# Performance work log

Measured on AMD Instinct MI355X. Metric: run time of the kernel, lower is better.

## Reference

```python
import jax, jax.numpy as jnp
import numpy as np

B, S, D, H, O = 8, 4096, 512, 512, 512
NS, NC, SD = 4, 4, 8
CLIP, TEMP, SUP_SCALE, SUP_EPS, LN_EPS = 3.0, 1.0, 1.0, 1e-4, 1e-5


def _ln(x, w, b):
    m = jnp.mean(x, -1, keepdims=True)
    v = jnp.mean((x - m) ** 2, -1, keepdims=True)
    return (x - m) * jax.lax.rsqrt(v + LN_EPS) * w + b


def _lin(x, w, b):
    return x @ w.T + b


def setup_inputs() -> dict:
    key = jax.random.key(0)
    ks = iter(jax.random.split(key, 32))

    def W(shape):
        return 0.02 * jax.random.normal(next(ks), shape, jnp.float32)

    inp = {}
    inp['x'] = jax.random.normal(next(ks), (B, S, D), jnp.float32)
    inp['sb_norm_w'] = jnp.ones((D,), jnp.float32)
    inp['sb_norm_b'] = jnp.zeros((D,), jnp.float32)
    inp['sb_proj_w'] = W((NS, D)); inp['sb_proj_b'] = jnp.zeros((NS,), jnp.float32)
    inp['sb_sum_w'] = W((SD, 4)); inp['sb_sum_b'] = jnp.zeros((SD,), jnp.float32)
    inp['cb_norm_w'] = jnp.ones((D,), jnp.float32)
    inp['cb_norm_b'] = jnp.zeros((D,), jnp.float32)
    inp['cb_proj_w'] = W((NC, D)); inp['cb_proj_b'] = jnp.zeros((NC,), jnp.float32)
    inp['cb_sum_w'] = W((SD, 4)); inp['cb_sum_b'] = jnp.zeros((SD,), jnp.float32)
    inp['vn_norm_w'] = jnp.ones((D,), jnp.float32)
    inp['vn_norm_b'] = jnp.zeros((D,), jnp.float32)
    inp['vn_w1'] = W((H, D)); inp['vn_b1'] = jnp.zeros((H,), jnp.float32)
    inp['vn_w2'] = W((O, H)); inp['vn_b2'] = jnp.zeros((O,), jnp.float32)
    inp['un_norm_w'] = jnp.ones((D,), jnp.float32)
    inp['un_norm_b'] = jnp.zeros((D,), jnp.float32)
    inp['un_w1'] = W((H, D)); inp['un_b1'] = jnp.zeros((H,), jnp.float32)
    inp['un_w2'] = W((1, H)); inp['un_b2'] = jnp.zeros((1,), jnp.float32)
    inp['en_w'] = W((H, 1)); inp['en_b'] = jnp.zeros((H,), jnp.float32)
    inp['pr_w'] = W((H, 1)); inp['pr_b'] = jnp.zeros((H,), jnp.float32)
    inp['rs_w'] = W((H, 1)); inp['rs_b'] = jnp.zeros((H,), jnp.float32)
    inp['ssp_w'] = W((H, SD)); inp['ssp_b'] = jnp.zeros((H,), jnp.float32)
    inp['csp_w'] = W((H, SD)); inp['csp_b'] = jnp.zeros((H,), jnp.float32)
    inp['out_w'] = W((O, O + 5 * H)); inp['out_b'] = jnp.zeros((O,), jnp.float32)
    inp['support_logits'] = jnp.zeros((NS,), jnp.float32)
    inp['conflict_weights'] = jnp.ones((NC,), jnp.float32)
    inp['drive_bias'] = jnp.zeros((1,), jnp.float32)
    inp['bias_resistance'] = jnp.zeros((1,), jnp.float32)
    inp['update_threshold'] = jnp.ones((1,), jnp.float32)
    inp['eml_gamma'] = jnp.full((1,), 0.3, jnp.float32)
    inp['eml_lambda'] = jnp.ones((1,), jnp.float32)
    inp['eml_bias'] = jnp.zeros((1,), jnp.float32)
    return inp


def reference(x, sb_norm_w, sb_norm_b, sb_proj_w, sb_proj_b, sb_sum_w, sb_sum_b,
              cb_norm_w, cb_norm_b, cb_proj_w, cb_proj_b, cb_sum_w, cb_sum_b,
              vn_norm_w, vn_norm_b, vn_w1, vn_b1, vn_w2, vn_b2,
              un_norm_w, un_norm_b, un_w1, un_b1, un_w2, un_b2,
              en_w, en_b, pr_w, pr_b, rs_w, rs_b,
              ssp_w, ssp_b, csp_w, csp_b, out_w, out_b,
              support_logits, conflict_weights, drive_bias, bias_resistance,
              update_threshold, eml_gamma, eml_lambda, eml_bias):
    # Support bank: LN -> Linear -> softplus(+eps) -> stats -> summary Linear
    sf = jax.nn.softplus(_lin(_ln(x, sb_norm_w, sb_norm_b), sb_proj_w, sb_proj_b)) + SUP_EPS  # [B,S,NS]
    ls = jnp.log(sf)
    s_seed = jnp.concatenate([
        sf.mean(-1, keepdims=True), sf.std(-1, keepdims=True),
        ls.mean(-1, keepdims=True), ls.max(-1, keepdims=True)], -1)
    ss = _lin(s_seed, sb_sum_w, sb_sum_b)  # [B,S,SD]
    # Conflict bank
    cf = jax.nn.softplus(_lin(_ln(x, cb_norm_w, cb_norm_b), cb_proj_w, cb_proj_b))  # [B,S,NC]
    c_seed = jnp.concatenate([
        cf.mean(-1, keepdims=True), cf.std(-1, keepdims=True),
        cf.max(-1, keepdims=True), cf.min(-1, keepdims=True)], -1)
    cs = _lin(c_seed, cb_sum_w, cb_sum_b)  # [B,S,SD]
    # Drive / resistance
    sw = jax.nn.softmax(support_logits)
    drive = drive_bias + SUP_SCALE * (ls * sw).sum(-1, keepdims=True) / np.sqrt(NS)
    cw = jax.nn.softplus(conflict_weights)
    weighted_conflict = (cf * cw).sum(-1, keepdims=True) / np.sqrt(NC)
    u_h = jax.nn.gelu(_lin(_ln(x, un_norm_w, un_norm_b), un_w1, un_b1), approximate=False)
    uncertainty = jax.nn.softplus(_lin(u_h, un_w2, un_b2))  # [B,S,1]
    resistance = bias_resistance + weighted_conflict + uncertainty
    # EML unit (dim=1): bounded linear drive-resistance balance, warmup_eta=1.0
    e_raw = eml_gamma * drive - eml_lambda * resistance + eml_bias
    energy = CLIP * jnp.tanh(e_raw / CLIP)
    activation = jax.nn.sigmoid(energy / TEMP)
    precision = jax.nn.softplus(energy - update_threshold)
    # Value net
    v_h = jax.nn.gelu(_lin(_ln(x, vn_norm_w, vn_norm_b), vn_w1, vn_b1), approximate=False)
    value = _lin(v_h, vn_w2, vn_b2)  # [B,S,O]
    feats = jnp.concatenate([
        activation * value,
        _lin(energy, en_w, en_b),
        _lin(precision, pr_w, pr_b),
        _lin(resistance, rs_w, rs_b),
        _lin(ss, ssp_w, ssp_b),
        _lin(cs, csp_w, csp_b)], -1)  # [B,S,O+5H]
    return _lin(feats, out_w, out_b)  # [B,S,O]
```

## Files before the change

kernel.cpp:

```cpp
#include <hip/hip_runtime.h>
#include <stdint.h>

typedef unsigned short u16;
typedef __bf16 bf16x8 __attribute__((ext_vector_type(8)));
typedef float f32x4 __attribute__((ext_vector_type(4)));
typedef __attribute__((address_space(1))) void gvoid;
typedef __attribute__((address_space(3))) void lvoid;

#define NTOK 32768

#define FENCE() asm volatile("" ::: "memory")
#define SBAR()  do { FENCE(); __builtin_amdgcn_s_barrier(); FENCE(); } while (0)
#define SVM4()  asm volatile("s_waitcnt vmcnt(4)" ::: "memory")
#define SVM0()  asm volatile("s_waitcnt vmcnt(0)" ::: "memory")

__device__ __forceinline__ u16 f2bf(float f) {
    unsigned u = __float_as_uint(f);
    u += 0x7fffu + ((u >> 16) & 1u);
    return (u16)(u >> 16);
}
__device__ __forceinline__ float softplusf(float x) {
    return fmaxf(x, 0.f) + log1pf(expf(-fabsf(x)));
}
__device__ __forceinline__ float geluf(float x) {
    return 0.5f * x * (1.f + erff(x * 0.7071067811865475f));
}
__device__ __forceinline__ float wave_sum(float v) {
#pragma unroll
    for (int o = 32; o > 0; o >>= 1) v += __shfl_xor(v, o);
    return v;
}
__device__ __forceinline__ float blk_sum(float v) {
    __shared__ float sm[4];
    v = wave_sum(v);
    __syncthreads();
    if ((threadIdx.x & 63) == 0) sm[threadIdx.x >> 6] = v;
    __syncthreads();
    return sm[0] + sm[1] + sm[2] + sm[3];
}

__global__ void k_fold(
    const float* __restrict__ vnw1, const float* __restrict__ vnnw, const float* __restrict__ vnnb, const float* __restrict__ vnb1,
    const float* __restrict__ unw1, const float* __restrict__ unnw, const float* __restrict__ unnb, const float* __restrict__ unb1,
    const float* __restrict__ sbpw, const float* __restrict__ sbpb, const float* __restrict__ sbnw, const float* __restrict__ sbnb,
    const float* __restrict__ cbpw, const float* __restrict__ cbpb, const float* __restrict__ cbnw, const float* __restrict__ cbnb,
    const float* __restrict__ outw, const float* __restrict__ enw, const float* __restrict__ enb,
    const float* __restrict__ prw, const float* __restrict__ prb,
    const float* __restrict__ rsw, const float* __restrict__ rsb,
    const float* __restrict__ sspw, const float* __restrict__ sspb,
    const float* __restrict__ cspw, const float* __restrict__ cspb,
    const float* __restrict__ vnw2, const float* __restrict__ vnb2,
    u16* __restrict__ Astk, float* __restrict__ bstk, float* __restrict__ pb,
    u16* __restrict__ Aow, u16* __restrict__ vnT,
    float* __restrict__ a_en, float* __restrict__ a_pr, float* __restrict__ a_rs,
    float* __restrict__ b_vo, float* __restrict__ c_cn, float* __restrict__ Mss, float* __restrict__ Mcs)
{
    const int b = blockIdx.x, t = threadIdx.x;
    if (b < 1024) {
        const float *w1, *nw, *nb; float bias;
        if (b < 512) { w1 = vnw1 + (size_t)b * 512; nw = vnnw; nb = vnnb; bias = vnb1[b]; }
        else { int r = b - 512; w1 = unw1 + (size_t)r * 512; nw = unnw; nb = unnb; bias = unb1[r]; }
        float part = 0.f;
        for (int d = t; d < 512; d += 256) {
            float wv = w1[d];
            Astk[(size_t)b * 512 + d] = f2bf(wv * nw[d]);
            part += wv * nb[d];
        }
        float s = blk_sum(part);
        if (t == 0) bstk[b] = bias + s;
    } else if (b < 1032) {
        int j = b - 1024;
        const float *pw, *nw, *nb; float bias;
        if (j < 4) { pw = sbpw + j * 512; nw = sbnw; nb = sbnb; bias = sbpb[j]; }
        else { pw = cbpw + (j - 4) * 512; nw = cbnw; nb = cbnb; bias = cbpb[j - 4]; }
        float part = 0.f;
        for (int d = t; d < 512; d += 256) {
            float wv = pw[d];
            Astk[(size_t)(1024 + j) * 512 + d] = f2bf(wv * nw[d]);
            part += wv * nb[d];
        }
        float s = blk_sum(part);
        if (t == 0) pb[j] = bias + s;
    } else if (b < 1152) {
        for (int d = t; d < 512; d += 256) Astk[(size_t)b * 512 + d] = 0;
    } else if (b < 1664) {
        int i = b - 1152;
        const float* ow = outw + (size_t)i * 3072;
        float pen = 0, ppr = 0, prs = 0, pbv = 0, pcc = 0;
        float pms[8], pmc[8];
#pragma unroll
        for (int k = 0; k < 8; k++) { pms[k] = 0.f; pmc[k] = 0.f; }
        for (int h = t; h < 512; h += 256) {
            float o0 = ow[h];        Aow[(size_t)i * 512 + h] = f2bf(o0); pbv += o0 * vnb2[h];
            float o1 = ow[512 + h];  pen += o1 * enw[h]; pcc += o1 * enb[h];
            float o2 = ow[1024 + h]; ppr += o2 * prw[h]; pcc += o2 * prb[h];
            float o3 = ow[1536 + h]; prs += o3 * rsw[h]; pcc += o3 * rsb[h];
            float o4 = ow[2048 + h]; pcc += o4 * sspb[h];
            float o5 = ow[2560 + h]; pcc += o5 * cspb[h];
#pragma unroll
            for (int k = 0; k < 8; k++) { pms[k] += o4 * sspw[h * 8 + k]; pmc[k] += o5 * cspw[h * 8 + k]; }
        }
        float r;
        r = blk_sum(pen); if (t == 0) a_en[i] = r;
        r = blk_sum(ppr); if (t == 0) a_pr[i] = r;
        r = blk_sum(prs); if (t == 0) a_rs[i] = r;
        r = blk_sum(pbv); if (t == 0) b_vo[i] = r;
        r = blk_sum(pcc); if (t == 0) c_cn[i] = r;
        for (int k = 0; k < 8; k++) { r = blk_sum(pms[k]); if (t == 0) Mss[i * 8 + k] = r; }
        for (int k = 0; k < 8; k++) { r = blk_sum(pmc[k]); if (t == 0) Mcs[i * 8 + k] = r; }
    } else {
        int hrow = b - 1664;
        for (int o = t; o < 512; o += 256)
            vnT[(size_t)hrow * 512 + o] = f2bf(vnw2[(size_t)o * 512 + hrow]);
    }
}

__device__ __forceinline__ void load_bfrag8(const u16* bufB, bf16x8 (&bfrag)[4][2], int wn, int l) {
#pragma unroll
    for (int nt = 0; nt < 4; nt++) {
        const int row = wn * 64 + nt * 16 + (l & 15);
#pragma unroll
        for (int ks = 0; ks < 2; ks++) {
            const int s = (ks * 4 + (l >> 4)) ^ (row & 7);
            bfrag[nt][ks] = *(const bf16x8*)(bufB + row * 64 + (s << 3));
        }
    }
}

template <int Q>
__device__ __forceinline__ void load_aquad8(const u16* bufA, bf16x8 (&af)[2], int wm, int l) {
    const int row = wm * 64 + Q * 16 + (l & 15);
#pragma unroll
    for (int ks = 0; ks < 2; ks++) {
        const int s = (ks * 4 + (l >> 4)) ^ (row & 7);
        af[ks] = *(const bf16x8*)(bufA + row * 64 + (s << 3));
    }
}

template <int Q>
__device__ __forceinline__ void do_mfma8(bf16x8 (&af)[2], bf16x8 (&bfrag)[4][2], f32x4 (&acc)[4][4]) {
#pragma unroll
    for (int nt = 0; nt < 4; nt++)
#pragma unroll
        for (int ks = 0; ks < 2; ks++)
            acc[Q][nt] = __builtin_amdgcn_mfma_f32_16x16x32_bf16(af[ks], bfrag[nt][ks], acc[Q][nt], 0, 0, 0);
}

#define PHASE8(Q, bufA_, bufB_, READB, STAGE_STMT, VM_STMT)       \
    do {                                                          \
        if (READB) load_bfrag8(bufB_, bfrag, wn, l);              \
        bf16x8 af[2];                                             \
        load_aquad8<Q>(bufA_, af, wm, l);                         \
        STAGE_STMT;                                               \
        SBAR();                                                   \
        __builtin_amdgcn_s_setprio(1);                            \
        do_mfma8<Q>(af, bfrag, acc);                              \
        __builtin_amdgcn_s_setprio(0);                            \
        VM_STMT;                                                  \
        SBAR();                                                   \
    } while (0)

__device__ __forceinline__ void gemm8_mainloop(const u16* __restrict__ Ag, const u16* __restrict__ Bg,
                                               size_t arow0, size_t brow0,
                                               u16* sm, f32x4 (&acc)[4][4], int w, int l)
{
    const int wm = w >> 1, wn = w & 1;
    u16* const sA0 = sm;
    u16* const sA1 = sm + 8192;
    u16* const sB0 = sm + 16384;
    u16* const sB1 = sm + 24576;
    const int rchunk = l >> 3;
    const int gc = (((l & 7) ^ ((l >> 3) & 7)) << 3);

    auto STG = [&](const u16* g, size_t rb, int tile, u16* lbase) {
        const int kt = tile * 64;
#pragma unroll
        for (int i = 0; i < 4; i++) {
            const int r0 = (w * 4 + i) * 8;
            __builtin_amdgcn_global_load_lds(
                (gvoid*)const_cast<u16*>(g + (rb + r0 + rchunk) * 512 + kt + gc),
                (lvoid*)(lbase + r0 * 64), 16, 0, 0);
        }
    };

    STG(Ag, arow0, 0, sA0);
    STG(Bg, brow0, 0, sB0);
    STG(Bg, brow0, 1, sB1);
    SVM4();
    SBAR();

    bf16x8 bfrag[4][2];
    for (int it = 0; it < 4; ++it) {
        const int t1 = 2 * it + 1, t2 = 2 * it + 2, t3 = 2 * it + 3;
        const bool lastit = (it == 3);
        PHASE8(0, sA0, sB0, true,  { STG(Ag, arow0, t1, sA1); }, );
        PHASE8(1, sA0, sB0, false, { if (t2 < 8) STG(Bg, brow0, t2, sB0); }, );
        PHASE8(2, sA0, sB0, false, { }, );
        PHASE8(3, sA0, sB0, false, { }, { if (lastit) { SVM0(); } else { SVM4(); } });
        PHASE8(0, sA1, sB1, true,  { if (t2 < 8) STG(Ag, arow0, t2, sA0); }, );
        PHASE8(1, sA1, sB1, false, { if (t3 < 8) STG(Bg, brow0, t3, sB1); }, );
        PHASE8(2, sA1, sB1, false, { }, );
        PHASE8(3, sA1, sB1, false, { }, { SVM4(); });
    }
}

__device__ __forceinline__ void gt_stage(const u16* __restrict__ A_, int lda,
                                         const u16* __restrict__ B_, int ldb, int kt,
                                         u16* dA, u16* dB, int w, int lrow, int lcol)
{
#pragma unroll
    for (int i = 0; i < 4; i++) {
        const int chunk = i * 4 + w;
        const int row = chunk * 8 + lrow;
        __builtin_amdgcn_global_load_lds((gvoid*)const_cast<u16*>(A_ + (size_t)row * lda + kt + lcol),
                                         (lvoid*)(dA + chunk * 512), 16, 0, 0);
        __builtin_amdgcn_global_load_lds((gvoid*)const_cast<u16*>(B_ + (size_t)row * ldb + kt + lcol),
                                         (lvoid*)(dB + chunk * 512), 16, 0, 0);
    }
}
__device__ __forceinline__ void gt_compute(const u16* lA, const u16* lB, f32x4 (&acc)[4][4],
                                           int wr, int wc, int frow, int fk, int sw)
{
#pragma unroll
    for (int ks = 0; ks < 2; ks++) {
        bf16x8 af[4], bfv[4];
        const int c = (ks * 32 + fk);
#pragma unroll
        for (int rt = 0; rt < 4; rt++)
            af[rt] = *(const bf16x8*)(lA + (wr + rt * 16 + frow) * 64 + (c ^ sw));
#pragma unroll
        for (int ct = 0; ct < 4; ct++)
            bfv[ct] = *(const bf16x8*)(lB + (wc + ct * 16 + frow) * 64 + (c ^ sw));
#pragma unroll
        for (int rt = 0; rt < 4; rt++)
#pragma unroll
            for (int ct = 0; ct < 4; ct++)
                acc[rt][ct] = __builtin_amdgcn_mfma_f32_16x16x32_bf16(af[rt], bfv[ct], acc[rt][ct], 0, 0, 0);
    }
}
__device__ __forceinline__ void gemm_tile(const u16* __restrict__ Ab, int lda,
                                          const u16* __restrict__ Bb, int ldb,
                                          int K, u16* sm, f32x4 (&acc)[4][4])
{
    const int t = threadIdx.x;
    const int w = t >> 6, l = t & 63;
    const int lrow = l >> 3;
    const int lcol = ((l ^ (((l >> 3) & 3) << 1)) & 7) * 8;
    const int wr = ((w >> 1) << 6), wc = ((w & 1) << 6);
    const int frow = l & 15, fk = ((l >> 4) << 3);
    const int sw = (frow & 3) << 4;
    u16* lA0 = sm;          u16* lA1 = sm + 8192;
    u16* lB0 = sm + 16384;  u16* lB1 = sm + 24576;
    gt_stage(Ab, lda, Bb, ldb, 0, lA0, lB0, w, lrow, lcol);
    __syncthreads();
    for (int kt = 0; kt < K; kt += 128) {
        if (kt + 64 < K) gt_stage(Ab, lda, Bb, ldb, kt + 64, lA1, lB1, w, lrow, lcol);
        gt_compute(lA0, lB0, acc, wr, wc, frow, fk, sw);
        __syncthreads();
        if (kt + 128 < K) gt_stage(Ab, lda, Bb, ldb, kt + 128, lA0, lB0, w, lrow, lcol);
        gt_compute(lA1, lB1, acc, wr, wc, frow, fk, sw);
        __syncthreads();
    }
}

__global__ __launch_bounds__(256, 2) void k_gemm_wvo(const u16* __restrict__ A, const u16* __restrict__ Bm,
                                                     u16* __restrict__ C)
{
    __shared__ __align__(16) u16 smem[32768];
    const f32x4 zero = {0.f, 0.f, 0.f, 0.f};
    f32x4 acc[4][4];
#pragma unroll
    for (int a = 0; a < 4; a++)
#pragma unroll
        for (int c = 0; c < 4; c++) acc[a][c] = zero;
    const u16* Ab = A + (size_t)blockIdx.y * 128 * 512;
    const u16* Bb = Bm + (size_t)blockIdx.x * 128 * 512;
    gemm_tile(Ab, 512, Bb, 512, 512, smem, acc);
    const int t = threadIdx.x, w = t >> 6, l = t & 63;
    const int rbase = blockIdx.y * 128 + ((w >> 1) << 6);
    const int cbase = blockIdx.x * 128 + ((w & 1) << 6);
    const int lr = ((l >> 4) << 2), lc = l & 15;
#pragma unroll
    for (int rt = 0; rt < 4; rt++)
#pragma unroll
        for (int ct = 0; ct < 4; ct++)
#pragma unroll
            for (int j = 0; j < 4; j++)
                C[(size_t)(rbase + rt * 16 + lr + j) * 512 + cbase + ct * 16 + lc] = f2bf(acc[rt][ct][j]);
}

__global__ void k_token(const float* __restrict__ x, u16* __restrict__ Ybf)
{
    const int w = threadIdx.x >> 6, l = threadIdx.x & 63;
    const int n = blockIdx.x * 4 + w;
    const float* xr = x + (size_t)n * 512;
    float4 xa = *(const float4*)(xr + 4 * l);
    float4 xb = *(const float4*)(xr + 256 + 4 * l);
    float v[8] = {xa.x, xa.y, xa.z, xa.w, xb.x, xb.y, xb.z, xb.w};
    float s1 = 0.f, s2 = 0.f;
#pragma unroll
    for (int c = 0; c < 8; c++) { s1 += v[c]; s2 += v[c] * v[c]; }
    s1 = wave_sum(s1); s2 = wave_sum(s2);
    const float mean = s1 * (1.f / 512.f);
    const float var = s2 * (1.f / 512.f) - mean * mean;
    const float rstd = rsqrtf(var + 1e-5f);
    float y[8];
#pragma unroll
    for (int c = 0; c < 8; c++) y[c] = (v[c] - mean) * rstd;
    *(ushort4*)(Ybf + (size_t)n * 512 + 4 * l) = make_ushort4(f2bf(y[0]), f2bf(y[1]), f2bf(y[2]), f2bf(y[3]));
    *(ushort4*)(Ybf + (size_t)n * 512 + 256 + 4 * l) = make_ushort4(f2bf(y[4]), f2bf(y[5]), f2bf(y[6]), f2bf(y[7]));
}

__global__ __launch_bounds__(256, 2) void k_gemm1(const u16* __restrict__ Y, const u16* __restrict__ Ast,
                                                  const float* __restrict__ bstk, const float* __restrict__ pb,
                                                  const float* __restrict__ unw2,
                                                  u16* __restrict__ H, float* __restrict__ wp,
                                                  float* __restrict__ wdotp)
{
    __shared__ __align__(16) u16 smem[32768];
    const f32x4 zero = {0.f, 0.f, 0.f, 0.f};
    f32x4 acc[4][4];
#pragma unroll
    for (int a = 0; a < 4; a++)
#pragma unroll
        for (int c = 0; c < 4; c++) acc[a][c] = zero;
    const int nwg = gridDim.x * gridDim.y;
    const int lin = blockIdx.y * gridDim.x + blockIdx.x;
    const int swz = (lin & 7) * (nwg >> 3) + (lin >> 3);
    const int by = swz / gridDim.x, bx = swz % gridDim.x;
    const int t = threadIdx.x, w = t >> 6, l = t & 63;

    gemm8_mainloop(Y, Ast, (size_t)by * 128, (size_t)bx * 128, smem, acc, w, l);

    const int wr = ((w >> 1) << 6), wc = ((w & 1) << 6);
    const int lr = ((l >> 4) << 2), lc = l & 15;
    if (bx == 8) {
        if ((w & 1) == 0 && lc < 8) {
            const float bv = pb[lc];
            const int rbase = by * 128 + wr;
#pragma unroll
            for (int rt = 0; rt < 4; rt++)
#pragma unroll
                for (int j = 0; j < 4; j++) {
                    const int n = rbase + rt * 16 + lr + j;
                    wp[(size_t)n * 8 + lc] = acc[rt][0][j] + bv;
                }
        }
        return;
    }
    if (bx >= 4) {
        const int cb = (bx - 4) * 128;
        float part[4][4];
#pragma unroll
        for (int rt = 0; rt < 4; rt++)
#pragma unroll
            for (int j = 0; j < 4; j++) part[rt][j] = 0.f;
#pragma unroll
        for (int ct = 0; ct < 4; ct++) {
            const int col = cb + wc + ct * 16 + lc;
            const float bv = bstk[512 + col];
            const float w2 = unw2[col];
#pragma unroll
            for (int rt = 0; rt < 4; rt++)
#pragma unroll
                for (int j = 0; j < 4; j++)
                    part[rt][j] += geluf(acc[rt][ct][j] + bv) * w2;
        }
        float* sf = (float*)smem;
        const int slot = ((w & 1) << 4) | lc;
        __syncthreads();
#pragma unroll
        for (int rt = 0; rt < 4; rt++)
#pragma unroll
            for (int j = 0; j < 4; j++)
                sf[(wr + rt * 16 + lr + j) * 32 + slot] = part[rt][j];
        __syncthreads();
        if (t < 128) {
            float s = 0.f;
#pragma unroll
            for (int k2 = 0; k2 < 32; k2++) s += sf[t * 32 + k2];
            wdotp[(size_t)(bx - 4) * NTOK + by * 128 + t] = s;
        }
        return;
    }
    __syncthreads();
#pragma unroll
    for (int ct = 0; ct < 4; ct++) {
        const int col = wc + ct * 16 + lc;
        const float bv = bstk[bx * 128 + col];
#pragma unroll
        for (int rt = 0; rt < 4; rt++) {
            const int row = wr + rt * 16 + lr;
#pragma unroll
            for (int j = 0; j < 4; j++)
                smem[(row + j) * 136 + col] = f2bf(geluf(acc[rt][ct][j] + bv));
        }
    }
    __syncthreads();
    const size_t gbase = (size_t)(by * 128) * 512 + bx * 128;
#pragma unroll
    for (int jj = 0; jj < 8; jj++) {
        const int r = jj * 16 + (t >> 4), u = t & 15;
        bf16x8 vv = *(const bf16x8*)(smem + r * 136 + u * 8);
        *(bf16x8*)(H + gbase + (size_t)r * 512 + u * 8) = vv;
    }
}

__global__ void k_bank(const float* __restrict__ wp, const float* __restrict__ wdotp,
                       const float* __restrict__ unb2,
                       const float* __restrict__ sbsw, const float* __restrict__ sbsb,
                       const float* __restrict__ cbsw, const float* __restrict__ cbsb,
                       const float* __restrict__ suplog, const float* __restrict__ confw,
                       const float* __restrict__ drvb, const float* __restrict__ biasres,
                       const float* __restrict__ emlg, const float* __restrict__ emll,
                       const float* __restrict__ emlb, const float* __restrict__ updthr,
                       float* __restrict__ wss, float* __restrict__ wcs, float* __restrict__ wsc)
{
    const int n = blockIdx.x * 256 + threadIdx.x;
    float4 p0 = *(const float4*)(wp + (size_t)n * 8);
    float4 p1 = *(const float4*)(wp + (size_t)n * 8 + 4);
    float p[8] = {p0.x, p0.y, p0.z, p0.w, p1.x, p1.y, p1.z, p1.w};
    const float dot = wdotp[n] + wdotp[NTOK + n] + wdotp[2 * NTOK + n] + wdotp[3 * NTOK + n];
    float sf[4], lsv[4], cf[4];
#pragma unroll
    for (int j = 0; j < 4; j++) {
        sf[j] = softplusf(p[j]) + 1e-4f;
        lsv[j] = logf(sf[j]);
        cf[j] = softplusf(p[j + 4]);
    }
    const float smn = 0.25f * (sf[0] + sf[1] + sf[2] + sf[3]);
    float sd = 0.f;
#pragma unroll
    for (int j = 0; j < 4; j++) sd += (sf[j] - smn) * (sf[j] - smn);
    const float sstd = sqrtf(0.25f * sd);
    const float lmn = 0.25f * (lsv[0] + lsv[1] + lsv[2] + lsv[3]);
    const float lmx = fmaxf(fmaxf(lsv[0], lsv[1]), fmaxf(lsv[2], lsv[3]));
    const float cmn = 0.25f * (cf[0] + cf[1] + cf[2] + cf[3]);
    float cd = 0.f;
#pragma unroll
    for (int j = 0; j < 4; j++) cd += (cf[j] - cmn) * (cf[j] - cmn);
    const float cstd = sqrtf(0.25f * cd);
    const float cmx = fmaxf(fmaxf(cf[0], cf[1]), fmaxf(cf[2], cf[3]));
    const float cmi = fminf(fminf(cf[0], cf[1]), fminf(cf[2], cf[3]));
    float seed_s[4] = {smn, sstd, lmn, lmx};
    float seed_c[4] = {cmn, cstd, cmx, cmi};
    float a4[8], b4[8];
#pragma unroll
    for (int k = 0; k < 8; k++) {
        float a = sbsb[k], b2 = cbsb[k];
#pragma unroll
        for (int j = 0; j < 4; j++) { a += sbsw[k * 4 + j] * seed_s[j]; b2 += cbsw[k * 4 + j] * seed_c[j]; }
        a4[k] = a; b4[k] = b2;
    }
    *(float4*)(wss + (size_t)n * 8)     = make_float4(a4[0], a4[1], a4[2], a4[3]);
    *(float4*)(wss + (size_t)n * 8 + 4) = make_float4(a4[4], a4[5], a4[6], a4[7]);
    *(float4*)(wcs + (size_t)n * 8)     = make_float4(b4[0], b4[1], b4[2], b4[3]);
    *(float4*)(wcs + (size_t)n * 8 + 4) = make_float4(b4[4], b4[5], b4[6], b4[7]);
    float mx = fmaxf(fmaxf(suplog[0], suplog[1]), fmaxf(suplog[2], suplog[3]));
    float e[4], se = 0.f;
#pragma unroll
    for (int j = 0; j < 4; j++) { e[j] = expf(suplog[j] - mx); se += e[j]; }
    float dv = 0.f, wcv = 0.f;
#pragma unroll
    for (int j = 0; j < 4; j++) { dv += lsv[j] * (e[j] / se); wcv += cf[j] * softplusf(confw[j]); }
    const float drive = drvb[0] + 0.5f * dv;
    const float unc = softplusf(dot + unb2[0]);
    const float res = biasres[0] + 0.5f * wcv + unc;
    const float er = emlg[0] * drive - emll[0] * res + emlb[0];
    const float energy = 3.f * tanhf(er * (1.f / 3.f));
    const float act = 1.f / (1.f + expf(-energy));
    const float prc = softplusf(energy - updthr[0]);
    wsc[(size_t)n * 4 + 0] = act;
    wsc[(size_t)n * 4 + 1] = energy;
    wsc[(size_t)n * 4 + 2] = prc;
    wsc[(size_t)n * 4 + 3] = res;
}

__global__ __launch_bounds__(256, 2) void k_gemm2(const u16* __restrict__ H, const u16* __restrict__ Wvo,
    const float* __restrict__ wsc, const float* __restrict__ wss, const float* __restrict__ wcs,
    const float* __restrict__ a_en, const float* __restrict__ a_pr, const float* __restrict__ a_rs,
    const float* __restrict__ b_vo, const float* __restrict__ c_cn,
    const float* __restrict__ Mss, const float* __restrict__ Mcs,
    const float* __restrict__ outb, float* __restrict__ out)
{
    __shared__ __align__(16) u16 smem[32768];
    const f32x4 zero = {0.f, 0.f, 0.f, 0.f};
    f32x4 acc[4][4];
#pragma unroll
    for (int a = 0; a < 4; a++)
#pragma unroll
        for (int c = 0; c < 4; c++) acc[a][c] = zero;
    const int nwg = gridDim.x * gridDim.y;
    const int lin = blockIdx.y * gridDim.x + blockIdx.x;
    const int swz = (lin & 7) * (nwg >> 3) + (lin >> 3);
    const int by = swz / gridDim.x, bx = swz % gridDim.x;
    const int t = threadIdx.x, w = t >> 6, l = t & 63;

    gemm8_mainloop(H, Wvo, (size_t)by * 128, (size_t)bx * 128, smem, acc, w, l);

    const int rbase = by * 128 + ((w >> 1) << 6);
    const int cbase = bx * 128 + ((w & 1) << 6);
    const int lr = ((l >> 4) << 2), lc = l & 15;
    float bvo4[4], aen4[4], apr4[4], ars4[4], cc4[4], ms4[4][8], mc4[4][8];
#pragma unroll
    for (int ct = 0; ct < 4; ct++) {
        const int i = cbase + ct * 16 + lc;
        bvo4[ct] = b_vo[i]; aen4[ct] = a_en[i]; apr4[ct] = a_pr[i]; ars4[ct] = a_rs[i];
        cc4[ct] = c_cn[i] + outb[i];
#pragma unroll
        for (int k = 0; k < 8; k++) { ms4[ct][k] = Mss[i * 8 + k]; mc4[ct][k] = Mcs[i * 8 + k]; }
    }
#pragma unroll
    for (int rt = 0; rt < 4; rt++)
#pragma unroll
        for (int j = 0; j < 4; j++) {
            const int n = rbase + rt * 16 + lr + j;
            const float act = wsc[(size_t)n * 4 + 0];
            const float eng = wsc[(size_t)n * 4 + 1];
            const float prc = wsc[(size_t)n * 4 + 2];
            const float res = wsc[(size_t)n * 4 + 3];
            float sv[8], cv[8];
#pragma unroll
            for (int k = 0; k < 8; k++) { sv[k] = wss[(size_t)n * 8 + k]; cv[k] = wcs[(size_t)n * 8 + k]; }
#pragma unroll
            for (int ct = 0; ct < 4; ct++) {
                const int i = cbase + ct * 16 + lc;
                float o = act * (acc[rt][ct][j] + bvo4[ct]) + eng * aen4[ct] + prc * apr4[ct]
                        + res * ars4[ct] + cc4[ct];
#pragma unroll
                for (int k = 0; k < 8; k++) o += ms4[ct][k] * sv[k] + mc4[ct][k] * cv[k];
                out[(size_t)n * 512 + i] = o;
            }
        }
}

extern "C" void kernel_launch(void* const* d_in, const int* in_sizes, int n_in,
                              void* d_out, int out_size, void* d_ws, size_t ws_size,
                              hipStream_t stream)
{
    const float* x       = (const float*)d_in[0];
    const float* sbnw    = (const float*)d_in[1];
    const float* sbnb    = (const float*)d_in[2];
    const float* sbpw    = (const float*)d_in[3];
    const float* sbpb    = (const float*)d_in[4];
    const float* sbsw    = (const float*)d_in[5];
    const float* sbsb    = (const float*)d_in[6];
    const float* cbnw    = (const float*)d_in[7];
    const float* cbnb    = (const float*)d_in[8];
    const float* cbpw    = (const float*)d_in[9];
    const float* cbpb    = (const float*)d_in[10];
    const float* cbsw    = (const float*)d_in[11];
    const float* cbsb    = (const float*)d_in[12];
    const float* vnnw    = (const float*)d_in[13];
    const float* vnnb    = (const float*)d_in[14];
    const float* vnw1    = (const float*)d_in[15];
    const float* vnb1    = (const float*)d_in[16];
    const float* vnw2    = (const float*)d_in[17];
    const float* vnb2    = (const float*)d_in[18];
    const float* unnw    = (const float*)d_in[19];
    const float* unnb    = (const float*)d_in[20];
    const float* unw1    = (const float*)d_in[21];
    const float* unb1    = (const float*)d_in[22];
    const float* unw2    = (const float*)d_in[23];
    const float* unb2    = (const float*)d_in[24];
    const float* enw     = (const float*)d_in[25];
    const float* enb     = (const float*)d_in[26];
    const float* prw     = (const float*)d_in[27];
    const float* prb     = (const float*)d_in[28];
    const float* rsw     = (const float*)d_in[29];
    const float* rsb     = (const float*)d_in[30];
    const float* sspw    = (const float*)d_in[31];
    const float* sspb    = (const float*)d_in[32];
    const float* cspw    = (const float*)d_in[33];
    const float* cspb    = (const float*)d_in[34];
    const float* outw    = (const float*)d_in[35];
    const float* outb    = (const float*)d_in[36];
    const float* suplog  = (const float*)d_in[37];
    const float* confw   = (const float*)d_in[38];
    const float* drvb    = (const float*)d_in[39];
    const float* biasres = (const float*)d_in[40];
    const float* updthr  = (const float*)d_in[41];
    const float* emlg    = (const float*)d_in[42];
    const float* emll    = (const float*)d_in[43];
    const float* emlb    = (const float*)d_in[44];
    float* out = (float*)d_out;
    (void)in_sizes; (void)n_in; (void)out_size; (void)ws_size;

    char* wsp = (char*)d_ws;
    size_t off = 0;
    auto alloc = [&](size_t bytes) { char* p = wsp + off; off = (off + bytes + 255) & ~(size_t)255; return p; };
    u16*  Ybf  = (u16*)alloc((size_t)NTOK * 512 * 2);
    u16*  Hbf  = (u16*)alloc((size_t)NTOK * 512 * 2);
    u16*  Astk = (u16*)alloc(1152 * 512 * 2);
    float* bstk = (float*)alloc(1024 * 4);
    float* pb   = (float*)alloc(8 * 4);
    u16*  Aow  = (u16*)alloc(512 * 512 * 2);
    u16*  vnT  = (u16*)alloc(512 * 512 * 2);
    u16*  Wvo  = (u16*)alloc(512 * 512 * 2);
    float* a_en = (float*)alloc(512 * 4);
    float* a_pr = (float*)alloc(512 * 4);
    float* a_rs = (float*)alloc(512 * 4);
    float* b_vo = (float*)alloc(512 * 4);
    float* c_cn = (float*)alloc(512 * 4);
    float* Mss  = (float*)alloc(512 * 8 * 4);
    float* Mcs  = (float*)alloc(512 * 8 * 4);
    float* wp   = (float*)alloc((size_t)NTOK * 8 * 4);
    float* wdotp= (float*)alloc((size_t)NTOK * 4 * 4);
    float* wss  = (float*)alloc((size_t)NTOK * 8 * 4);
    float* wcs  = (float*)alloc((size_t)NTOK * 8 * 4);
    float* wsc  = (float*)alloc((size_t)NTOK * 4 * 4);

    k_fold<<<2176, 256, 0, stream>>>(vnw1, vnnw, vnnb, vnb1, unw1, unnw, unnb, unb1,
                                     sbpw, sbpb, sbnw, sbnb, cbpw, cbpb, cbnw, cbnb,
                                     outw, enw, enb, prw, prb, rsw, rsb, sspw, sspb, cspw, cspb,
                                     vnw2, vnb2,
                                     Astk, bstk, pb, Aow, vnT, a_en, a_pr, a_rs, b_vo, c_cn, Mss, Mcs);
    k_gemm_wvo<<<dim3(4, 4), 256, 0, stream>>>(Aow, vnT, Wvo);
    k_token<<<NTOK / 4, 256, 0, stream>>>(x, Ybf);
    k_gemm1<<<dim3(9, 256), 256, 0, stream>>>(Ybf, Astk, bstk, pb, unw2, Hbf, wp, wdotp);
    k_bank<<<NTOK / 256, 256, 0, stream>>>(wp, wdotp, unb2, sbsw, sbsb, cbsw, cbsb,
                                           suplog, confw, drvb, biasres, emlg, emll, emlb, updthr,
                                           wss, wcs, wsc);
    k_gemm2<<<dim3(4, 256), 256, 0, stream>>>(Hbf, Wvo, wsc, wss, wcs, a_en, a_pr, a_rs, b_vo, c_cn,
                                              Mss, Mcs, outb, out);
}
```

Before: 154.1 us.

## Fuse Wvo weight GEMM into gemm1 grid and bank math into gemm2 prologue

The small Wvo = Aow·vnT GEMM becomes an extra grid column in k_gemm1 (bx==9, 16 active blocks), and the separate k_bank kernel is dropped. Its per-token math is recomputed into shared memory at the start of each k_gemm2 block. This removes two kernel launches and the global round-trip of the wss/wcs/wsc intermediates. In exchange, the bank computation is done redundantly by each of the 4 column blocks, 240 extra blocks launch and exit at once, and k_gemm2 uses more LDS, which could reduce occupancy.

```diff
diff --git a/kernel.cpp b/kernel.cpp
--- a/kernel.cpp
+++ b/kernel.cpp
@@ -204,91 +204,6 @@
     }
 }
 
-__device__ __forceinline__ void gt_stage(const u16* __restrict__ A_, int lda,
-                                         const u16* __restrict__ B_, int ldb, int kt,
-                                         u16* dA, u16* dB, int w, int lrow, int lcol)
-{
-#pragma unroll
-    for (int i = 0; i < 4; i++) {
-        const int chunk = i * 4 + w;
-        const int row = chunk * 8 + lrow;
-        __builtin_amdgcn_global_load_lds((gvoid*)const_cast<u16*>(A_ + (size_t)row * lda + kt + lcol),
-                                         (lvoid*)(dA + chunk * 512), 16, 0, 0);
-        __builtin_amdgcn_global_load_lds((gvoid*)const_cast<u16*>(B_ + (size_t)row * ldb + kt + lcol),
-                                         (lvoid*)(dB + chunk * 512), 16, 0, 0);
-    }
-}
-__device__ __forceinline__ void gt_compute(const u16* lA, const u16* lB, f32x4 (&acc)[4][4],
-                                           int wr, int wc, int frow, int fk, int sw)
-{
-#pragma unroll
-    for (int ks = 0; ks < 2; ks++) {
-        bf16x8 af[4], bfv[4];
-        const int c = (ks * 32 + fk);
-#pragma unroll
-        for (int rt = 0; rt < 4; rt++)
-            af[rt] = *(const bf16x8*)(lA + (wr + rt * 16 + frow) * 64 + (c ^ sw));
-#pragma unroll
-        for (int ct = 0; ct < 4; ct++)
-            bfv[ct] = *(const bf16x8*)(lB + (wc + ct * 16 + frow) * 64 + (c ^ sw));
-#pragma unroll
-        for (int rt = 0; rt < 4; rt++)
-#pragma unroll
-            for (int ct = 0; ct < 4; ct++)
-                acc[rt][ct] = __builtin_amdgcn_mfma_f32_16x16x32_bf16(af[rt], bfv[ct], acc[rt][ct], 0, 0, 0);
-    }
-}
-__device__ __forceinline__ void gemm_tile(const u16* __restrict__ Ab, int lda,
-                                          const u16* __restrict__ Bb, int ldb,
-                                          int K, u16* sm, f32x4 (&acc)[4][4])
-{
-    const int t = threadIdx.x;
-    const int w = t >> 6, l = t & 63;
-    const int lrow = l >> 3;
-    const int lcol = ((l ^ (((l >> 3) & 3) << 1)) & 7) * 8;
-    const int wr = ((w >> 1) << 6), wc = ((w & 1) << 6);
-    const int frow = l & 15, fk = ((l >> 4) << 3);
-    const int sw = (frow & 3) << 4;
-    u16* lA0 = sm;          u16* lA1 = sm + 8192;
-    u16* lB0 = sm + 16384;  u16* lB1 = sm + 24576;
-    gt_stage(Ab, lda, Bb, ldb, 0, lA0, lB0, w, lrow, lcol);
-    __syncthreads();
-    for (int kt = 0; kt < K; kt += 128) {
-        if (kt + 64 < K) gt_stage(Ab, lda, Bb, ldb, kt + 64, lA1, lB1, w, lrow, lcol);
-        gt_compute(lA0, lB0, acc, wr, wc, frow, fk, sw);
-        __syncthreads();
-        if (kt + 128 < K) gt_stage(Ab, lda, Bb, ldb, kt + 128, lA0, lB0, w, lrow, lcol);
-        gt_compute(lA1, lB1, acc, wr, wc, frow, fk, sw);
-        __syncthreads();
-    }
-}
-
-__global__ __launch_bounds__(256, 2) void k_gemm_wvo(const u16* __restrict__ A, const u16* __restrict__ Bm,
-                                                     u16* __restrict__ C)
-{
-    __shared__ __align__(16) u16 smem[32768];
-    const f32x4 zero = {0.f, 0.f, 0.f, 0.f};
-    f32x4 acc[4][4];
-#pragma unroll
-    for (int a = 0; a < 4; a++)
-#pragma unroll
-        for (int c = 0; c < 4; c++) acc[a][c] = zero;
-    const u16* Ab = A + (size_t)blockIdx.y * 128 * 512;
-    const u16* Bb = Bm + (size_t)blockIdx.x * 128 * 512;
-    gemm_tile(Ab, 512, Bb, 512, 512, smem, acc);
-    const int t = threadIdx.x, w = t >> 6, l = t & 63;
-    const int rbase = blockIdx.y * 128 + ((w >> 1) << 6);
-    const int cbase = blockIdx.x * 128 + ((w & 1) << 6);
-    const int lr = ((l >> 4) << 2), lc = l & 15;
-#pragma unroll
-    for (int rt = 0; rt < 4; rt++)
-#pragma unroll
-        for (int ct = 0; ct < 4; ct++)
-#pragma unroll
-            for (int j = 0; j < 4; j++)
-                C[(size_t)(rbase + rt * 16 + lr + j) * 512 + cbase + ct * 16 + lc] = f2bf(acc[rt][ct][j]);
-}
-
 __global__ void k_token(const float* __restrict__ x, u16* __restrict__ Ybf)
 {
     const int w = threadIdx.x >> 6, l = threadIdx.x & 63;
@@ -314,6 +229,8 @@
 __global__ __launch_bounds__(256, 2) void k_gemm1(const u16* __restrict__ Y, const u16* __restrict__ Ast,
                                                   const float* __restrict__ bstk, const float* __restrict__ pb,
                                                   const float* __restrict__ unw2,
+                                                  const u16* __restrict__ Aow, const u16* __restrict__ vnT,
+                                                  u16* __restrict__ Wvo,
                                                   u16* __restrict__ H, float* __restrict__ wp,
                                                   float* __restrict__ wdotp)
 {
@@ -329,11 +246,26 @@
     const int swz = (lin & 7) * (nwg >> 3) + (lin >> 3);
     const int by = swz / gridDim.x, bx = swz % gridDim.x;
     const int t = threadIdx.x, w = t >> 6, l = t & 63;
-
-    gemm8_mainloop(Y, Ast, (size_t)by * 128, (size_t)bx * 128, smem, acc, w, l);
-
     const int wr = ((w >> 1) << 6), wc = ((w & 1) << 6);
     const int lr = ((l >> 4) << 2), lc = l & 15;
+
+    if (bx == 9) {
+        if (by >= 16) return;
+        gemm8_mainloop(Aow, vnT, (size_t)(by >> 2) * 128, (size_t)(by & 3) * 128, smem, acc, w, l);
+        const int rbase = (by >> 2) * 128 + wr;
+        const int cbase = (by & 3) * 128 + wc;
+#pragma unroll
+        for (int rt = 0; rt < 4; rt++)
+#pragma unroll
+            for (int ct = 0; ct < 4; ct++)
+#pragma unroll
+                for (int j = 0; j < 4; j++)
+                    Wvo[(size_t)(rbase + rt * 16 + lr + j) * 512 + cbase + ct * 16 + lc] = f2bf(acc[rt][ct][j]);
+        return;
+    }
+
+    gemm8_mainloop(Y, Ast, (size_t)by * 128, (size_t)bx * 128, smem, acc, w, l);
+
     if (bx == 8) {
         if ((w & 1) == 0 && lc < 8) {
             const float bv = pb[lc];
@@ -406,84 +338,22 @@
     }
 }
 
-__global__ void k_bank(const float* __restrict__ wp, const float* __restrict__ wdotp,
-                       const float* __restrict__ unb2,
-                       const float* __restrict__ sbsw, const float* __restrict__ sbsb,
-                       const float* __restrict__ cbsw, const float* __restrict__ cbsb,
-                       const float* __restrict__ suplog, const float* __restrict__ confw,
-                       const float* __restrict__ drvb, const float* __restrict__ biasres,
-                       const float* __restrict__ emlg, const float* __restrict__ emll,
-                       const float* __restrict__ emlb, const float* __restrict__ updthr,
-                       float* __restrict__ wss, float* __restrict__ wcs, float* __restrict__ wsc)
-{
-    const int n = blockIdx.x * 256 + threadIdx.x;
-    float4 p0 = *(const float4*)(wp + (size_t)n * 8);
-    float4 p1 = *(const float4*)(wp + (size_t)n * 8 + 4);
-    float p[8] = {p0.x, p0.y, p0.z, p0.w, p1.x, p1.y, p1.z, p1.w};
-    const float dot = wdotp[n] + wdotp[NTOK + n] + wdotp[2 * NTOK + n] + wdotp[3 * NTOK + n];
-    float sf[4], lsv[4], cf[4];
-#pragma unroll
-    for (int j = 0; j < 4; j++) {
-        sf[j] = softplusf(p[j]) + 1e-4f;
-        lsv[j] = logf(sf[j]);
-        cf[j] = softplusf(p[j + 4]);
-    }
-    const float smn = 0.25f * (sf[0] + sf[1] + sf[2] + sf[3]);
-    float sd = 0.f;
-#pragma unroll
-    for (int j = 0; j < 4; j++) sd += (sf[j] - smn) * (sf[j] - smn);
-    const float sstd = sqrtf(0.25f * sd);
-    const float lmn = 0.25f * (lsv[0] + lsv[1] + lsv[2] + lsv[3]);
-    const float lmx = fmaxf(fmaxf(lsv[0], lsv[1]), fmaxf(lsv[2], lsv[3]));
-    const float cmn = 0.25f * (cf[0] + cf[1] + cf[2] + cf[3]);
-    float cd = 0.f;
-#pragma unroll
-    for (int j = 0; j < 4; j++) cd += (cf[j] - cmn) * (cf[j] - cmn);
-    const float cstd = sqrtf(0.25f * cd);
-    const float cmx = fmaxf(fmaxf(cf[0], cf[1]), fmaxf(cf[2], cf[3]));
-    const float cmi = fminf(fminf(cf[0], cf[1]), fminf(cf[2], cf[3]));
-    float seed_s[4] = {smn, sstd, lmn, lmx};
-    float seed_c[4] = {cmn, cstd, cmx, cmi};
-    float a4[8], b4[8];
-#pragma unroll
-    for (int k = 0; k < 8; k++) {
-        float a = sbsb[k], b2 = cbsb[k];
-#pragma unroll
-        for (int j = 0; j < 4; j++) { a += sbsw[k * 4 + j] * seed_s[j]; b2 += cbsw[k * 4 + j] * seed_c[j]; }
-        a4[k] = a; b4[k] = b2;
-    }
-    *(float4*)(wss + (size_t)n * 8)     = make_float4(a4[0], a4[1], a4[2], a4[3]);
-    *(float4*)(wss + (size_t)n * 8 + 4) = make_float4(a4[4], a4[5], a4[6], a4[7]);
-    *(float4*)(wcs + (size_t)n * 8)     = make_float4(b4[0], b4[1], b4[2], b4[3]);
-    *(float4*)(wcs + (size_t)n * 8 + 4) = make_float4(b4[4], b4[5], b4[6], b4[7]);
-    float mx = fmaxf(fmaxf(suplog[0], suplog[1]), fmaxf(suplog[2], suplog[3]));
-    float e[4], se = 0.f;
-#pragma unroll
-    for (int j = 0; j < 4; j++) { e[j] = expf(suplog[j] - mx); se += e[j]; }
-    float dv = 0.f, wcv = 0.f;
-#pragma unroll
-    for (int j = 0; j < 4; j++) { dv += lsv[j] * (e[j] / se); wcv += cf[j] * softplusf(confw[j]); }
-    const float drive = drvb[0] + 0.5f * dv;
-    const float unc = softplusf(dot + unb2[0]);
-    const float res = biasres[0] + 0.5f * wcv + unc;
-    const float er = emlg[0] * drive - emll[0] * res + emlb[0];
-    const float energy = 3.f * tanhf(er * (1.f / 3.f));
-    const float act = 1.f / (1.f + expf(-energy));
-    const float prc = softplusf(energy - updthr[0]);
-    wsc[(size_t)n * 4 + 0] = act;
-    wsc[(size_t)n * 4 + 1] = energy;
-    wsc[(size_t)n * 4 + 2] = prc;
-    wsc[(size_t)n * 4 + 3] = res;
-}
-
 __global__ __launch_bounds__(256, 2) void k_gemm2(const u16* __restrict__ H, const u16* __restrict__ Wvo,
-    const float* __restrict__ wsc, const float* __restrict__ wss, const float* __restrict__ wcs,
+    const float* __restrict__ wp, const float* __restrict__ wdotp,
+    const float* __restrict__ unb2,
+    const float* __restrict__ sbsw, const float* __restrict__ sbsb,
+    const float* __restrict__ cbsw, const float* __restrict__ cbsb,
+    const float* __restrict__ suplog, const float* __restrict__ confw,
+    const float* __restrict__ drvb, const float* __restrict__ biasres,
+    const float* __restrict__ emlg, const float* __restrict__ emll,
+    const float* __restrict__ emlb, const float* __restrict__ updthr,
     const float* __restrict__ a_en, const float* __restrict__ a_pr, const float* __restrict__ a_rs,
     const float* __restrict__ b_vo, const float* __restrict__ c_cn,
     const float* __restrict__ Mss, const float* __restrict__ Mcs,
     const float* __restrict__ outb, float* __restrict__ out)
 {
     __shared__ __align__(16) u16 smem[32768];
+    __shared__ float sbank[128 * 20];
     const f32x4 zero = {0.f, 0.f, 0.f, 0.f};
     f32x4 acc[4][4];
 #pragma unroll
@@ -496,9 +366,65 @@
     const int by = swz / gridDim.x, bx = swz % gridDim.x;
     const int t = threadIdx.x, w = t >> 6, l = t & 63;
 
+    if (t < 128) {
+        const int n = by * 128 + t;
+        float4 p0 = *(const float4*)(wp + (size_t)n * 8);
+        float4 p1 = *(const float4*)(wp + (size_t)n * 8 + 4);
+        float p[8] = {p0.x, p0.y, p0.z, p0.w, p1.x, p1.y, p1.z, p1.w};
+        const float dot = wdotp[n] + wdotp[NTOK + n] + wdotp[2 * NTOK + n] + wdotp[3 * NTOK + n];
+        float sf[4], lsv[4], cf[4];
+#pragma unroll
+        for (int j = 0; j < 4; j++) {
+            sf[j] = softplusf(p[j]) + 1e-4f;
+            lsv[j] = logf(sf[j]);
+            cf[j] = softplusf(p[j + 4]);
+        }
+        const float smn = 0.25f * (sf[0] + sf[1] + sf[2] + sf[3]);
+        float sd = 0.f;
+#pragma unroll
+        for (int j = 0; j < 4; j++) sd += (sf[j] - smn) * (sf[j] - smn);
+        const float sstd = sqrtf(0.25f * sd);
+        const float lmn = 0.25f * (lsv[0] + lsv[1] + lsv[2] + lsv[3]);
+        const float lmx = fmaxf(fmaxf(lsv[0], lsv[1]), fmaxf(lsv[2], lsv[3]));
+        const float cmn = 0.25f * (cf[0] + cf[1] + cf[2] + cf[3]);
+        float cd = 0.f;
+#pragma unroll
+        for (int j = 0; j < 4; j++) cd += (cf[j] - cmn) * (cf[j] - cmn);
+        const float cstd = sqrtf(0.25f * cd);
+        const float cmx = fmaxf(fmaxf(cf[0], cf[1]), fmaxf(cf[2], cf[3]));
+        const float cmi = fminf(fminf(cf[0], cf[1]), fminf(cf[2], cf[3]));
+        float seed_s[4] = {smn, sstd, lmn, lmx};
+        float seed_c[4] = {cmn, cstd, cmx, cmi};
+#pragma unroll
+        for (int k = 0; k < 8; k++) {
+            float a = sbsb[k], b2 = cbsb[k];
+#pragma unroll
+            for (int j = 0; j < 4; j++) { a += sbsw[k * 4 + j] * seed_s[j]; b2 += cbsw[k * 4 + j] * seed_c[j]; }
+            sbank[t * 20 + 4 + k] = a;
+            sbank[t * 20 + 12 + k] = b2;
+        }
+        float mx = fmaxf(fmaxf(suplog[0], suplog[1]), fmaxf(suplog[2], suplog[3]));
+        float e[4], se = 0.f;
+#pragma unroll
+        for (int j = 0; j < 4; j++) { e[j] = expf(suplog[j] - mx); se += e[j]; }
+        float dv = 0.f, wcv = 0.f;
+#pragma unroll
+        for (int j = 0; j < 4; j++) { dv += lsv[j] * (e[j] / se); wcv += cf[j] * softplusf(confw[j]); }
+        const float drive = drvb[0] + 0.5f * dv;
+        const float unc = softplusf(dot + unb2[0]);
+        const float res = biasres[0] + 0.5f * wcv + unc;
+        const float er = emlg[0] * drive - emll[0] * res + emlb[0];
+        const float energy = 3.f * tanhf(er * (1.f / 3.f));
+        sbank[t * 20 + 0] = 1.f / (1.f + expf(-energy));
+        sbank[t * 20 + 1] = energy;
+        sbank[t * 20 + 2] = softplusf(energy - updthr[0]);
+        sbank[t * 20 + 3] = res;
+    }
+    __syncthreads();
+
     gemm8_mainloop(H, Wvo, (size_t)by * 128, (size_t)bx * 128, smem, acc, w, l);
 
-    const int rbase = by * 128 + ((w >> 1) << 6);
+    const int rl0 = ((w >> 1) << 6);
     const int cbase = bx * 128 + ((w & 1) << 6);
     const int lr = ((l >> 4) << 2), lc = l & 15;
     float bvo4[4], aen4[4], apr4[4], ars4[4], cc4[4], ms4[4][8], mc4[4][8];
@@ -514,22 +440,21 @@
     for (int rt = 0; rt < 4; rt++)
 #pragma unroll
         for (int j = 0; j < 4; j++) {
-            const int n = rbase + rt * 16 + lr + j;
-            const float act = wsc[(size_t)n * 4 + 0];
-            const float eng = wsc[(size_t)n * 4 + 1];
-            const float prc = wsc[(size_t)n * 4 + 2];
-            const float res = wsc[(size_t)n * 4 + 3];
-            float sv[8], cv[8];
-#pragma unroll
-            for (int k = 0; k < 8; k++) { sv[k] = wss[(size_t)n * 8 + k]; cv[k] = wcs[(size_t)n * 8 + k]; }
+            const int nl = rl0 + rt * 16 + lr + j;
+            const size_t n = (size_t)by * 128 + nl;
+            const float act = sbank[nl * 20 + 0];
+            const float eng = sbank[nl * 20 + 1];
+            const float prc = sbank[nl * 20 + 2];
+            const float res = sbank[nl * 20 + 3];
 #pragma unroll
             for (int ct = 0; ct < 4; ct++) {
                 const int i = cbase + ct * 16 + lc;
                 float o = act * (acc[rt][ct][j] + bvo4[ct]) + eng * aen4[ct] + prc * apr4[ct]
                         + res * ars4[ct] + cc4[ct];
 #pragma unroll
-                for (int k = 0; k < 8; k++) o += ms4[ct][k] * sv[k] + mc4[ct][k] * cv[k];
-                out[(size_t)n * 512 + i] = o;
+                for (int k = 0; k < 8; k++)
+                    o += ms4[ct][k] * sbank[nl * 20 + 4 + k] + mc4[ct][k] * sbank[nl * 20 + 12 + k];
+                out[n * 512 + i] = o;
             }
         }
 }
@@ -606,21 +531,16 @@
     float* Mcs  = (float*)alloc(512 * 8 * 4);
     float* wp   = (float*)alloc((size_t)NTOK * 8 * 4);
     float* wdotp= (float*)alloc((size_t)NTOK * 4 * 4);
-    float* wss  = (float*)alloc((size_t)NTOK * 8 * 4);
-    float* wcs  = (float*)alloc((size_t)NTOK * 8 * 4);
-    float* wsc  = (float*)alloc((size_t)NTOK * 4 * 4);
 
     k_fold<<<2176, 256, 0, stream>>>(vnw1, vnnw, vnnb, vnb1, unw1, unnw, unnb, unb1,
                                      sbpw, sbpb, sbnw, sbnb, cbpw, cbpb, cbnw, cbnb,
                                      outw, enw, enb, prw, prb, rsw, rsb, sspw, sspb, cspw, cspb,
                                      vnw2, vnb2,
                                      Astk, bstk, pb, Aow, vnT, a_en, a_pr, a_rs, b_vo, c_cn, Mss, Mcs);
-    k_gemm_wvo<<<dim3(4, 4), 256, 0, stream>>>(Aow, vnT, Wvo);
     k_token<<<NTOK / 4, 256, 0, stream>>>(x, Ybf);
-    k_gemm1<<<dim3(9, 256), 256, 0, stream>>>(Ybf, Astk, bstk, pb, unw2, Hbf, wp, wdotp);
-    k_bank<<<NTOK / 256, 256, 0, stream>>>(wp, wdotp, unb2, sbsw, sbsb, cbsw, cbsb,
-                                           suplog, confw, drvb, biasres, emlg, emll, emlb, updthr,
-                                           wss, wcs, wsc);
-    k_gemm2<<<dim3(4, 256), 256, 0, stream>>>(Hbf, Wvo, wsc, wss, wcs, a_en, a_pr, a_rs, b_vo, c_cn,
-                                              Mss, Mcs, outb, out);
-}
+    k_gemm1<<<dim3(10, 256), 256, 0, stream>>>(Ybf, Astk, bstk, pb, unw2, Aow, vnT, Wvo,
+                                               Hbf, wp, wdotp);
+    k_gemm2<<<dim3(4, 256), 256, 0, stream>>>(Hbf, Wvo, wp, wdotp, unb2, sbsw, sbsb, cbsw, cbsb,
+                                              suplog, confw, drvb, biasres, emlg, emll, emlb, updthr,
+                                              a_en, a_pr, a_rs, b_vo, c_cn, Mss, Mcs, outb, out);
+}
```

New measurement: 153.0 us. Within noise of the previous version (-0.7%).
